# Optimization experiments

Hardware: AMD Instinct MI355X
Metric: run time of the kernel (lower is better)

## Reference

```python
import jax, jax.numpy as jnp
import numpy as np

MUL = 32          # multiplicity per irrep
NB = 10           # number_of_basis
MAX_R = 4.0
NUM_NEIGH = 16.0
NUM_NODES = 512.0
N_GRAPHS = 16
N = 8192
E = 131072
L = 3             # gated layers
C_S = float(np.sin(np.pi / 8))
C_X = float(np.cos(np.pi / 8))
SQ3 = float(np.sqrt(3.0))
SQ2 = float(np.sqrt(2.0))


def smooth_cutoff(x):
    u = 2.0 * (x - 1.0)
    y = 0.5 * (1.0 - jnp.cos(np.pi * u))
    return jnp.where(u > 0.0, 0.0, jnp.where(u < -1.0, 1.0, y))


def radial_embed(r):
    # soft_one_hot_linspace, basis='gaussian', cutoff=False, scaled by sqrt(NB)
    values = jnp.linspace(0.0, MAX_R, NB)
    step = values[1] - values[0]
    diff = (r[:, None] - values[None, :]) / step
    return jnp.exp(-diff * diff) / 1.12 * np.sqrt(NB)


def _lin_s(a, w):  # scalar-channel linear with e3nn fan-in norm
    return (a @ w) / np.sqrt(w.shape[0])


def _lin_v(a, w):  # vector-channel (l=1) linear, acts on multiplicity only
    return jnp.einsum('nui,uv->nvi', a, w) / np.sqrt(w.shape[0])


def forward(x, edge_vec, lin1_so, lin1_se, lin1_vo, lin1_ve,
            sc_so, sc_se, sc_vo, sc_ve, rad_w1, rad_w2,
            lin2_so, lin2_se, lin2_vo, lin2_ve,
            flin1_se, flin1_vo, fsc_se, frad_w1, frad_w2, flin2,
            edge_src, edge_dst, batch):
    n = x.shape[0]
    M = MUL
    # split node features into irrep blocks: 32x0o + 32x0e + 32x1o + 32x1e
    s_o = x[:, :M]
    s_e = x[:, M:2 * M]
    v_o = x[:, 2 * M:5 * M].reshape(n, M, 3)
    v_e = x[:, 5 * M:8 * M].reshape(n, M, 3)

    r = jnp.linalg.norm(edge_vec, axis=1)
    unit = edge_vec / (r[:, None] + 1e-12)
    cut = smooth_cutoff(r / MAX_R)          # [E]
    y0 = cut                                # l=0 edge attr (Y0 = 1, component norm)
    y1 = SQ3 * unit * cut[:, None]          # l=1 edge attr, [E,3]
    emb = radial_embed(r)                   # [E,NB]

    def seg(v):
        return jax.ops.segment_sum(v, edge_dst, num_segments=n) / np.sqrt(NUM_NEIGH)

    inv2 = 1.0 / np.sqrt(2.0)  # path normalization: 2 tp paths into output irrep
    inv3 = 1.0 / np.sqrt(3.0)  # 3 tp paths into output irrep

    def layer(carry, p):
        s_o, s_e, v_o, v_e = carry
        (w1so, w1se, w1vo, w1ve, wsso, wsse, wsvo, wsve,
         rw1, rw2, w2so, w2se, w2vo, w2ve) = p
        # lin1 (FullyConnectedTensorProduct with trivial node attr == per-irrep linear)
        a_so, a_se = _lin_s(s_o, w1so), _lin_s(s_e, w1se)
        a_vo, a_ve = _lin_v(v_o, w1vo), _lin_v(v_e, w1ve)
        e_so, e_se = a_so[edge_src], a_se[edge_src]
        e_vo, e_ve = a_vo[edge_src], a_ve[edge_src]
        # radial MLP -> per-edge tensor-product weights (10 uvu paths x MUL)
        h = jax.nn.silu(emb @ rw1 / np.sqrt(NB))
        w = (h @ rw2 / np.sqrt(rw1.shape[1])).reshape(-1, 10, M)
        # explicit lmax=1 Clebsch-Gordan contractions
        dot_ve = jnp.einsum('eui,ei->eu', e_ve, y1) / SQ3   # 1e x 1o -> 0o
        dot_vo = jnp.einsum('eui,ei->eu', e_vo, y1) / SQ3   # 1o x 1o -> 0e
        cr_ve = jnp.cross(e_ve, y1[:, None, :]) / SQ2       # 1e x 1o -> 1o
        cr_vo = jnp.cross(e_vo, y1[:, None, :]) / SQ2       # 1o x 1o -> 1e
        m0o = jnp.concatenate([w[:, 0] * e_so * y0[:, None],
                               w[:, 1] * dot_ve], axis=1) * inv2          # [E,2M]
        m0e = jnp.concatenate([w[:, 2] * e_se * y0[:, None],
                               w[:, 3] * dot_vo], axis=1) * inv2          # [E,2M]
        m1o = jnp.concatenate([w[:, 4][:, :, None] * e_se[:, :, None] * y1[:, None, :],
                               w[:, 5][:, :, None] * e_vo * y0[:, None, None],
                               w[:, 6][:, :, None] * cr_ve], axis=1) * inv3  # [E,3M,3]
        m1e = jnp.concatenate([w[:, 7][:, :, None] * e_so[:, :, None] * y1[:, None, :],
                               w[:, 8][:, :, None] * cr_vo,
                               w[:, 9][:, :, None] * e_ve * y0[:, None, None]], axis=1) * inv3
        n0o, n0e, n1o, n1e = seg(m0o), seg(m0e), seg(m1o), seg(m1e)
        # lin2 plus self-connection skip: sin(pi/8)*sc + cos(pi/8)*conv
        o0o = C_S * _lin_s(s_o, wsso) + C_X * _lin_s(n0o, w2so)   # [N,M]
        o0e = C_S * _lin_s(s_e, wsse) + C_X * _lin_s(n0e, w2se)   # [N,3M] (M scalars + 2M gates)
        o1o = C_S * _lin_v(v_o, wsvo) + C_X * _lin_v(n1o, w2vo)   # [N,M,3]
        o1e = C_S * _lin_v(v_e, wsve) + C_X * _lin_v(n1e, w2ve)   # [N,M,3]
        # Gate: tanh on 0o scalars, silu on 0e scalars, sigmoid gates on vectors
        ns_o = jnp.tanh(o0o)
        ns_e = jax.nn.silu(o0e[:, :M])
        g = jax.nn.sigmoid(o0e[:, M:])
        nv_o = o1o * g[:, :M, None]
        nv_e = o1e * g[:, M:, None]
        return (ns_o, ns_e, nv_o, nv_e), None

    (s_o, s_e, v_o, v_e), _ = jax.lax.scan(
        layer, (s_o, s_e, v_o, v_e),
        (lin1_so, lin1_se, lin1_vo, lin1_ve, sc_so, sc_se, sc_vo, sc_ve,
         rad_w1, rad_w2, lin2_so, lin2_se, lin2_vo, lin2_ve))

    # final convolution -> 1x0e (paths: 0e x 0e -> 0e, 1o x 1o -> 0e)
    a_se = _lin_s(s_e, flin1_se)
    a_vo = _lin_v(v_o, flin1_vo)
    h = jax.nn.silu(emb @ frad_w1 / np.sqrt(NB))
    w = (h @ frad_w2 / np.sqrt(frad_w1.shape[1])).reshape(-1, 2, MUL)
    dot_vo = jnp.einsum('eui,ei->eu', a_vo[edge_src], y1) / SQ3
    m0e = jnp.concatenate([w[:, 0] * a_se[edge_src] * y0[:, None],
                           w[:, 1] * dot_vo], axis=1) * inv2
    n0e = seg(m0e)
    out = C_S * _lin_s(s_e, fsc_se) + C_X * _lin_s(n0e, flin2)   # [N,1]
    # reduce_output: per-graph sum / sqrt(num_nodes)
    return jax.ops.segment_sum(out, batch, num_segments=N_GRAPHS) / np.sqrt(NUM_NODES)


def setup_inputs():
    key = jax.random.key(0)
    ks = jax.random.split(key, 26)
    rn = lambda k, s: jax.random.normal(k, s, dtype=jnp.float32)
    M = MUL
    return {
        "x": rn(ks[0], (N, 8 * M)),
        "edge_vec": rn(ks[1], (E, 3)),
        "lin1_so": rn(ks[2], (L, M, M)),
        "lin1_se": rn(ks[3], (L, M, M)),
        "lin1_vo": rn(ks[4], (L, M, M)),
        "lin1_ve": rn(ks[5], (L, M, M)),
        "sc_so": rn(ks[6], (L, M, M)),
        "sc_se": rn(ks[7], (L, M, 3 * M)),
        "sc_vo": rn(ks[8], (L, M, M)),
        "sc_ve": rn(ks[9], (L, M, M)),
        "rad_w1": rn(ks[10], (L, NB, 100)),
        "rad_w2": rn(ks[11], (L, 100, 10 * M)),
        "lin2_so": rn(ks[12], (L, 2 * M, M)),
        "lin2_se": rn(ks[13], (L, 2 * M, 3 * M)),
        "lin2_vo": rn(ks[14], (L, 3 * M, M)),
        "lin2_ve": rn(ks[15], (L, 3 * M, M)),
        "flin1_se": rn(ks[16], (M, M)),
        "flin1_vo": rn(ks[17], (M, M)),
        "fsc_se": rn(ks[18], (M, 1)),
        "frad_w1": rn(ks[19], (NB, 100)),
        "frad_w2": rn(ks[20], (100, 2 * M)),
        "flin2": rn(ks[21], (2 * M, 1)),
        "edge_src": jax.random.randint(ks[22], (E,), 0, N),
        "edge_dst": jax.random.randint(ks[23], (E,), 0, N),
        "batch": jnp.sort(jax.random.randint(ks[24], (N,), 0, N_GRAPHS)),
    }


def reference(x, edge_vec, lin1_so, lin1_se, lin1_vo, lin1_ve,
              sc_so, sc_se, sc_vo, sc_ve, rad_w1, rad_w2,
              lin2_so, lin2_se, lin2_vo, lin2_ve,
              flin1_se, flin1_vo, fsc_se, frad_w1, frad_w2, flin2,
              edge_src, edge_dst, batch):
    return forward(x, edge_vec, lin1_so, lin1_se, lin1_vo, lin1_ve,
                   sc_so, sc_se, sc_vo, sc_ve, rad_w1, rad_w2,
                   lin2_so, lin2_se, lin2_vo, lin2_ve,
                   flin1_se, flin1_vo, fsc_se, frad_w1, frad_w2, flin2,
                   edge_src, edge_dst, batch)
```

## Files before the change

### kernel.cpp

```cpp
#include <hip/hip_runtime.h>
#include <hip/hip_bf16.h>
#include <math.h>
#include <string.h>
#include <stdint.h>

#define NN 8192
#define EE 131072

#define PI_F     3.14159265358979323846f
#define SQRT3_F  1.7320508075688772f
#define INV_SQ2  0.7071067811865476f
#define INV_SQ3  0.5773502691896258f
#define INV_S32  0.17677669529663687f
#define INV_S96  0.10206207261596575f
#define INV_S10  0.31622776601683794f
#define C_S_F    0.3826834323650898f
#define C_X_F    0.9238795325112867f
#define EMB_S    2.8234621965789795f
#define OUT_S    0.044194173824159216f

typedef unsigned int uint;
typedef unsigned short ushort;
typedef unsigned long long u64;
typedef __attribute__((ext_vector_type(8))) short short8;
typedef __attribute__((ext_vector_type(4))) float float4v;

__device__ __forceinline__ float sigmoid_f(float x){ return 1.0f/(1.0f+__expf(-x)); }
__device__ __forceinline__ ushort f2bf(float f){
    uint u = __float_as_uint(f);
    u = (u + 0x7fffu + ((u>>16)&1u)) >> 16;
    return (ushort)u;
}
__device__ __forceinline__ float bf2f(ushort w){ return __uint_as_float(((uint)w)<<16); }
__device__ __forceinline__ uint pk2bf(float a, float b){
    __hip_bfloat162 h = __float22bfloat162_rn(make_float2(a,b));
    uint u; memcpy(&u,&h,4); return u;
}

__global__ __launch_bounds__(256) void k_count(const int* __restrict__ dst, int* __restrict__ cnt)
{
    int e = blockIdx.x*256 + threadIdx.x;
    atomicAdd(&cnt[dst[e]], 1);
}

__global__ __launch_bounds__(1024) void k_scan(const int* __restrict__ cnt,
    int* __restrict__ off, int* __restrict__ cur)
{
    __shared__ int partial[1024];
    int t = threadIdx.x;
    int base = t*8;
    int local[8];
    int s = 0;
    #pragma unroll
    for(int i=0;i<8;i++){ local[i]=s; s += cnt[base+i]; }
    partial[t] = s;
    __syncthreads();
    for(int d=1; d<1024; d<<=1){
        int v = (t>=d) ? partial[t-d] : 0;
        __syncthreads();
        partial[t] += v;
        __syncthreads();
    }
    int pref = (t>0) ? partial[t-1] : 0;
    #pragma unroll
    for(int i=0;i<8;i++){
        int o = pref + local[i];
        off[base+i] = o; cur[base+i] = o;
    }
    if (t==1023) off[NN] = partial[1023];
}

__global__ __launch_bounds__(256) void k_scatter(const int* __restrict__ dst,
    int* __restrict__ cur, int* __restrict__ eids)
{
    int e = blockIdx.x*256 + threadIdx.x;
    int p = atomicAdd(&cur[dst[e]], 1);
    eids[p] = e;
}

__global__ __launch_bounds__(256) void k_geom_sorted(const float* __restrict__ ev,
    const int* __restrict__ eids, const int* __restrict__ esrc,
    const int* __restrict__ edst, const int* __restrict__ batch,
    float4* __restrict__ ygeo, float* __restrict__ embs,
    int* __restrict__ esrcs, int* __restrict__ gbs)
{
    int p = blockIdx.x*256 + threadIdx.x;
    int e = eids[p];
    float vx=ev[e*3+0], vy=ev[e*3+1], vz=ev[e*3+2];
    float r = sqrtf(vx*vx+vy*vy+vz*vz);
    float uu = 0.5f*r - 2.0f;
    float cut;
    if (uu > 0.0f)       cut = 0.0f;
    else if (uu < -1.0f) cut = 1.0f;
    else                 cut = 0.5f*(1.0f - cosf(PI_F*uu));
    float s = SQRT3_F*cut/(r + 1e-12f);
    ygeo[p] = make_float4(cut, vx*s, vy*s, vz*s);
    #pragma unroll
    for(int b=0;b<10;b++){
        float d = r*2.25f - (float)b;
        embs[p*10+b] = __expf(-d*d)*EMB_S;
    }
    esrcs[p] = esrc[e];
    gbs[p]   = batch[edst[e]];
}

__global__ __launch_bounds__(256) void k_lin1(const float* __restrict__ st,
    const float* __restrict__ w_so, const float* __restrict__ w_se,
    const float* __restrict__ w_vo, const float* __restrict__ w_ve,
    uint* __restrict__ Abf)
{
    __shared__ float wl[4][1024];
    __shared__ float sl[8][256];
    __shared__ float ol[8][256];
    int t = threadIdx.x;
    for(int i=t;i<1024;i+=256){ wl[0][i]=w_so[i]; wl[1][i]=w_se[i]; wl[2][i]=w_vo[i]; wl[3][i]=w_ve[i]; }
    int n0 = blockIdx.x*8;
    for(int i=t;i<2048;i+=256){ int k=i>>8, c=i&255; sl[k][c]=st[(n0+k)*256+c]; }
    __syncthreads();
    for(int k=0;k<8;k++){
        float acc = 0.0f;
        if (t < 64){
            int m = t>>5, v = t&31;
            const float* w = wl[m];
            const float* s = &sl[k][m*32];
            #pragma unroll
            for(int u=0;u<32;u++) acc += s[u]*w[u*32+v];
        } else if (t < 160){
            int idx=t-64, i=idx>>5, v=idx&31;
            #pragma unroll
            for(int u=0;u<32;u++) acc += sl[k][64+u*3+i]*wl[2][u*32+v];
        } else {
            int idx=t-160, i=idx>>5, v=idx&31;
            #pragma unroll
            for(int u=0;u<32;u++) acc += sl[k][160+u*3+i]*wl[3][u*32+v];
        }
        ol[k][t] = acc * INV_S32;
    }
    __syncthreads();
    for(int idx=t; idx<1024; idx+=256){
        int k = idx>>7, j = idx&127, q = j>>5, u = j&31;
        Abf[(size_t)(n0+k)*128 + j] = pk2bf(ol[k][q*64 + u], ol[k][q*64 + 32 + u]);
    }
}

__global__ __launch_bounds__(256) void k_prep3(const float* __restrict__ rw2, ushort* __restrict__ Bfrag)
{
    int L = blockIdx.x / 160;
    int idx = (blockIdx.x % 160)*256 + threadIdx.x;
    int j = idx & 7;
    int l = (idx>>3) & 63;
    int rest = idx >> 9;
    int nt = rest % 20;
    int ks = rest / 20;
    int k = ks*32 + ((l>>4)&3)*8 + j;
    int p = nt*16 + (l&15);
    int n = (2*(p>>6) + (p&1))*32 + ((p&63)>>1);
    float v = (k < 100) ? rw2[L*32000 + k*320 + n] : 0.0f;
    Bfrag[L*40960 + idx] = f2bf(v);
}

__global__ __launch_bounds__(256) void k_prep64(const float* __restrict__ rw2, ushort* __restrict__ Bfrag)
{
    int idx = blockIdx.x*256 + threadIdx.x;
    int j = idx & 7;
    int l = (idx>>3) & 63;
    int rest = idx >> 9;
    int nt = rest % 4;
    int ks = rest / 4;
    int k = ks*32 + ((l>>4)&3)*8 + j;
    int p = nt*16 + (l&15);
    int n = (p % 2)*32 + p/2;
    float v = (k < 100) ? rw2[k*64 + n] : 0.0f;
    Bfrag[idx] = f2bf(v);
}

__global__ __launch_bounds__(256) void k_prepu(
    const float* __restrict__ sc_so, const float* __restrict__ sc_se,
    const float* __restrict__ sc_vo, const float* __restrict__ sc_ve,
    const float* __restrict__ lin2_so, const float* __restrict__ lin2_se,
    const float* __restrict__ lin2_vo, const float* __restrict__ lin2_ve,
    float* __restrict__ Wcat0, float* __restrict__ Wcat1)
{
    int idx = blockIdx.x*256 + threadIdx.x;
    int L = idx / 20480;
    int k = idx % 20480;
    const float CS32 = C_S_F*INV_S32, CX8 = C_X_F*0.125f, CX96 = C_X_F*INV_S96;
    if (k < 12288){
        int r = k >> 7, c = k & 127;
        float v;
        if (c < 32) v = (r<32) ? CS32*sc_so[L*1024 + r*32+c]        : CX8*lin2_so[L*2048 + (r-32)*32+c];
        else        v = (r<32) ? CS32*sc_se[L*3072 + r*96+(c-32)]   : CX8*lin2_se[L*6144 + (r-32)*96+(c-32)];
        Wcat0[L*12288 + k] = v;
    } else {
        int k2 = k - 12288;
        int r = k2 >> 6, c = k2 & 63;
        float v;
        if (c < 32) v = (r<32) ? CS32*sc_vo[L*1024 + r*32+c]        : CX96*lin2_vo[L*3072 + (r-32)*32+c];
        else        v = (r<32) ? CS32*sc_ve[L*1024 + r*32+(c-32)]   : CX96*lin2_ve[L*3072 + (r-32)*32+(c-32)];
        Wcat1[L*8192 + k2] = v;
    }
}

template<int NCOL>
__global__ __launch_bounds__(256, 3) void k_radial_mfma(const float* __restrict__ emb,
    const float* __restrict__ rw1, const ushort* __restrict__ Afrag,
    ushort* __restrict__ Wout)
{
    constexpr int MTW = NCOL/64;
    constexpr int STR = NCOL + 8;
    constexpr int BIG = (64*STR > 8192) ? 64*STR : 8192;
    __shared__ __align__(16) ushort s_big[BIG];
    __shared__ float s_emb[640];
    int t = threadIdx.x;
    int ebase = blockIdx.x*64;
    for(int i=t;i<640;i+=256)  s_emb[i] = emb[ebase*10 + i];
    for(int i=t;i<1024;i+=256) ((uint*)s_big)[3072 + i] = 0u;
    __syncthreads();
    {
        int w4 = __builtin_amdgcn_readfirstlane(t) >> 6;
        int l = t & 63;
        float ev[10];
        #pragma unroll
        for(int r=0;r<10;r++) ev[r] = s_emb[l*10 + r];
        int m  = l & 15, nt = l >> 4;
        int kbeg = w4*25;
        #pragma unroll 5
        for(int k=kbeg; k<kbeg+25; k++){
            float a0 = 0.0f;
            #pragma unroll
            for(int r=0;r<10;r++) a0 += ev[r]*rw1[r*100 + k];
            a0 *= INV_S10;
            float h = a0*sigmoid_f(a0);
            int ks = k >> 5, kk = k & 31;
            int lt = m | ((kk>>3)<<4);
            s_big[((ks*4 + nt)*64 + lt)*8 + (kk&7)] = f2bf(h);
        }
    }
    __syncthreads();
    int w = t >> 6, l = t & 63;
    float4v acc[MTW][4];
    #pragma unroll
    for(int a=0;a<MTW;a++)
        #pragma unroll
        for(int b=0;b<4;b++)
            acc[a][b] = (float4v){0.f,0.f,0.f,0.f};
    #pragma unroll
    for(int ks=0;ks<4;ks++){
        short8 bfr[4];
        #pragma unroll
        for(int nt=0;nt<4;nt++)
            bfr[nt] = *((const short8*)&s_big[((ks*4+nt)*64 + l)*8]);
        #pragma unroll
        for(int mtl=0;mtl<MTW;mtl++){
            short8 af = *((const short8*)(Afrag + ((size_t)(ks*(NCOL/16) + w*MTW + mtl)*64 + l)*8));
            #pragma unroll
            for(int nt=0;nt<4;nt++)
                acc[mtl][nt] = __builtin_amdgcn_mfma_f32_16x16x32_bf16(af, bfr[nt], acc[mtl][nt], 0, 0, 0);
        }
    }
    __syncthreads();
    {
        int col16 = l & 15, rquad = l >> 4;
        #pragma unroll
        for(int mtl=0;mtl<MTW;mtl++){
            int pos0 = (w*MTW + mtl)*16 + rquad*4;
            #pragma unroll
            for(int nt=0;nt<4;nt++){
                int edge = nt*16 + col16;
                uint u01 = pk2bf(acc[mtl][nt][0]*0.1f, acc[mtl][nt][1]*0.1f);
                uint u23 = pk2bf(acc[mtl][nt][2]*0.1f, acc[mtl][nt][3]*0.1f);
                u64 pk = (u64)u01 | ((u64)u23 << 32);
                *((u64*)&s_big[edge*STR + pos0]) = pk;
            }
        }
    }
    __syncthreads();
    for (int idx = t; idx < 64*(NCOL/8); idx += 256){
        int row = idx/(NCOL/8), o8 = idx%(NCOL/8);
        short8 vv = *((const short8*)&s_big[row*STR + o8*8]);
        *((short8*)(Wout + (size_t)(ebase+row)*NCOL + o8*8)) = vv;
    }
}

__global__ __launch_bounds__(64) void k_aggregate(const uint* __restrict__ Abf,
    const ushort* __restrict__ W2, const float4* __restrict__ ygeo,
    const int* __restrict__ off, const int* __restrict__ esrcs,
    float* __restrict__ nbuf)
{
    int n = blockIdx.x;
    int l = threadIdx.x;
    int u = l & 31, half = l >> 5;
    int e0 = off[n], e1 = off[n+1];
    float a_n0o0=0.f, a_n0o1=0.f, a_n0e0=0.f, a_n0e1=0.f;
    float a1o[3][3] = {{0}}, a1e[3][3] = {{0}};
    #pragma unroll 2
    for(int p=e0;p<e1;p+=2){
        int idx = p + half;
        bool valid = idx < e1;
        int ic = valid ? idx : e0;
        int s = esrcs[ic];
        float4 yg = ygeo[ic];
        float cy0 = valid ? yg.x : 0.0f;
        float v1x = yg.y, v1y = yg.z, v1z = yg.w;
        if (!valid){ v1x=0.f; v1y=0.f; v1z=0.f; }
        const uint* Au = Abf + (size_t)s*128;
        uint a01=Au[u], a23=Au[32+u], a45=Au[64+u], a67=Au[96+u];
        float aso=bf2f((ushort)a01), ase=bf2f((ushort)(a01>>16));
        float vox=bf2f((ushort)a23), voy=bf2f((ushort)(a23>>16));
        float voz=bf2f((ushort)a45), vex=bf2f((ushort)(a45>>16));
        float vey=bf2f((ushort)a67), vez=bf2f((ushort)(a67>>16));
        const uint* Wu = (const uint*)(W2) + (size_t)ic*160;
        uint p01=Wu[u], p23=Wu[32+u], p45=Wu[64+u], p67=Wu[96+u], p89=Wu[128+u];
        float w0=bf2f((ushort)p01), w1=bf2f((ushort)(p01>>16));
        float w2=bf2f((ushort)p23), w3=bf2f((ushort)(p23>>16));
        float w4=bf2f((ushort)p45), w5=bf2f((ushort)(p45>>16));
        float w6=bf2f((ushort)p67), w7=bf2f((ushort)(p67>>16));
        float w8=bf2f((ushort)p89), w9=bf2f((ushort)(p89>>16));
        float dve = (vex*v1x+vey*v1y+vez*v1z)*INV_SQ3;
        float dvo = (vox*v1x+voy*v1y+voz*v1z)*INV_SQ3;
        float cvex=(vey*v1z-vez*v1y)*INV_SQ2, cvey=(vez*v1x-vex*v1z)*INV_SQ2, cvez=(vex*v1y-vey*v1x)*INV_SQ2;
        float cvox=(voy*v1z-voz*v1y)*INV_SQ2, cvoy=(voz*v1x-vox*v1z)*INV_SQ2, cvoz=(vox*v1y-voy*v1x)*INV_SQ2;
        a_n0o0 += w0*aso*cy0;
        a_n0o1 += w1*dve;
        a_n0e0 += w2*ase*cy0;
        a_n0e1 += w3*dvo;
        a1o[0][0]+=w4*ase*v1x; a1o[0][1]+=w4*ase*v1y; a1o[0][2]+=w4*ase*v1z;
        a1o[1][0]+=w5*vox*cy0; a1o[1][1]+=w5*voy*cy0; a1o[1][2]+=w5*voz*cy0;
        a1o[2][0]+=w6*cvex;    a1o[2][1]+=w6*cvey;    a1o[2][2]+=w6*cvez;
        a1e[0][0]+=w7*aso*v1x; a1e[0][1]+=w7*aso*v1y; a1e[0][2]+=w7*aso*v1z;
        a1e[1][0]+=w8*cvox;    a1e[1][1]+=w8*cvoy;    a1e[1][2]+=w8*cvoz;
        a1e[2][0]+=w9*vex*cy0; a1e[2][1]+=w9*vey*cy0; a1e[2][2]+=w9*vez*cy0;
    }
    a_n0o0 += __shfl_xor(a_n0o0, 32);
    a_n0o1 += __shfl_xor(a_n0o1, 32);
    a_n0e0 += __shfl_xor(a_n0e0, 32);
    a_n0e1 += __shfl_xor(a_n0e1, 32);
    #pragma unroll
    for(int sp=0;sp<3;sp++)
        #pragma unroll
        for(int i=0;i<3;i++){
            a1o[sp][i] += __shfl_xor(a1o[sp][i], 32);
            a1e[sp][i] += __shfl_xor(a1e[sp][i], 32);
        }
    float s0 = INV_SQ2*0.25f;
    float s1 = INV_SQ3*0.25f;
    float* nb = nbuf + n*704;
    if (half==0){
        nb[u]      = a_n0o0*s0;
        nb[32+u]   = a_n0o1*s0;
        nb[64+u]   = a_n0e0*s0;
        nb[96+u]   = a_n0e1*s0;
        #pragma unroll
        for(int sp=0;sp<3;sp++)
            #pragma unroll
            for(int i=0;i<3;i++)
                nb[128 + i*96 + sp*32 + u] = a1o[sp][i]*s1;
    } else {
        #pragma unroll
        for(int sp=0;sp<3;sp++)
            #pragma unroll
            for(int i=0;i<3;i++)
                nb[416 + i*96 + sp*32 + u] = a1e[sp][i]*s1;
    }
}

__global__ __launch_bounds__(256, 4) void k_update(const float* __restrict__ st,
    const float* __restrict__ nbuf, const float* __restrict__ W0,
    const float* __restrict__ W1, float* __restrict__ stnew)
{
    __shared__ float X0T[192][8];
    __shared__ float X1T[3][256][8];
    __shared__ float G[8][64];
    int t = threadIdx.x;
    int n0 = blockIdx.x*8;
    for (int idx=t; idx<2048; idx+=256){
        int nb = idx>>8, c = idx&255;
        float v = st[(n0+nb)*256 + c];
        if (c<32)       X0T[c][nb]=v;
        else if (c<64)  X0T[96+(c-32)][nb]=v;
        else if (c<160){ int cc=c-64;  X1T[cc%3][cc/3][nb]=v; }
        else           { int cc=c-160; X1T[cc%3][128+cc/3][nb]=v; }
    }
    for (int idx=t; idx<5632; idx+=256){
        int nb = idx/704, o = idx%704;
        float v = nbuf[(n0+nb)*704 + o];
        if (o<64)       X0T[32+o][nb]=v;
        else if (o<128) X0T[128+(o-64)][nb]=v;
        else if (o<416){ int oo=o-128; X1T[oo/96][32+(oo%96)][nb]=v; }
        else           { int oo=o-416; X1T[oo/96][160+(oo%96)][nb]=v; }
    }
    __syncthreads();
    {
        int c = t & 127, h = t >> 7;
        float a0=0.f,a1=0.f,a2=0.f,a3=0.f;
        int qb = (c<32) ? 0 : 96;
        #pragma unroll 4
        for (int r=0;r<96;r++){
            float w = W0[r*128+c];
            const float* xp = &X0T[qb+r][h*4];
            a0 += w*xp[0]; a1 += w*xp[1]; a2 += w*xp[2]; a3 += w*xp[3];
        }
        float accs[4]={a0,a1,a2,a3};
        #pragma unroll
        for (int j=0;j<4;j++){
            int nb = h*4+j, n = n0+nb;
            float o = accs[j];
            if (c<32)       stnew[n*256+c] = tanhf(o);
            else if (c<64)  stnew[n*256+c] = o*sigmoid_f(o);
            else            G[nb][c-64] = sigmoid_f(o);
        }
    }
    __syncthreads();
    int c2 = t & 63, w = t >> 6;
    if (w < 3){
        float acc[8];
        #pragma unroll
        for(int j=0;j<8;j++) acc[j]=0.f;
        int qb = (c2<32) ? 0 : 128;
        #pragma unroll 2
        for (int r=0;r<128;r++){
            float wt = W1[r*64+c2];
            const float* xp = &X1T[w][qb+r][0];
            #pragma unroll
            for(int j=0;j<8;j++) acc[j] += wt*xp[j];
        }
        int base = (c2<32) ? 64 + c2*3 + w : 160 + (c2-32)*3 + w;
        #pragma unroll
        for(int j=0;j<8;j++)
            stnew[(n0+j)*256 + base] = acc[j]*G[j][c2];
    }
}

__global__ __launch_bounds__(128) void k_flin(const float* __restrict__ st,
    const float* __restrict__ wse, const float* __restrict__ wvo,
    const float* __restrict__ fsc_se,
    float* __restrict__ afin, float* __restrict__ sk)
{
    int n = blockIdx.x, t = threadIdx.x;
    const float* sr = st + n*256;
    float acc = 0.0f;
    if (t < 32){
        #pragma unroll
        for(int u=0;u<32;u++) acc += sr[32+u]*wse[u*32+t];
    } else {
        int idx=t-32, i=idx>>5, v=idx&31;
        #pragma unroll
        for(int u=0;u<32;u++) acc += sr[64+u*3+i]*wvo[u*32+v];
    }
    afin[n*128 + t] = acc * INV_S32;
    if (t < 32){
        float v = sr[32+t]*fsc_se[t];
        #pragma unroll
        for(int o=16;o>0;o>>=1) v += __shfl_xor(v, o);
        if (t==0) sk[n] = v * (C_S_F*INV_S32*OUT_S);
    }
}

__global__ __launch_bounds__(256) void k_fagg(const float* __restrict__ afin,
    const ushort* __restrict__ Wf2, const int* __restrict__ esrcs,
    const float4* __restrict__ ygeo, const int* __restrict__ gbs,
    const float* __restrict__ flin2, float* __restrict__ fpart)
{
    __shared__ float s_g[16];
    int t = threadIdx.x;
    if (t < 16) s_g[t] = 0.0f;
    __syncthreads();
    int u = t & 31, half = (t>>5)&1, w = t >> 6;
    const float FACT = C_X_F*0.125f*INV_SQ2*0.25f*OUT_S;
    float fl0 = flin2[u], fl1 = flin2[32+u];
    int base = (blockIdx.x*4 + w)*64;
    #pragma unroll 2
    for(int it=0; it<32; it++){
        int idx = base + it*2 + half;
        int s = esrcs[idx];
        float4 yg = ygeo[idx];
        const float* Ar = afin + s*128;
        float ase = Ar[u];
        float vx=Ar[32+u], vy=Ar[64+u], vz=Ar[96+u];
        uint p01 = *((const uint*)(Wf2 + (size_t)idx*64 + u*2));
        float w0 = bf2f((ushort)p01), w1 = bf2f((ushort)(p01>>16));
        float val = fl0*w0*ase*yg.x + fl1*w1*((vx*yg.y+vy*yg.z+vz*yg.w)*INV_SQ3);
        #pragma unroll
        for(int o=16;o>0;o>>=1) val += __shfl_xor(val, o);
        if (u==0) atomicAdd(&s_g[gbs[idx]], val*FACT);
    }
    __syncthreads();
    if (t < 16) fpart[blockIdx.x*16 + t] = s_g[t];
}

__global__ __launch_bounds__(256) void k_final(const float* __restrict__ sk,
    const int* __restrict__ batch, const float* __restrict__ fpart,
    float* __restrict__ out)
{
    __shared__ float bins[16];
    int t = threadIdx.x, b = blockIdx.x;
    if (t < 16) bins[t] = 0.0f;
    __syncthreads();
    if (t < 128){
        int n = b*128 + t;
        atomicAdd(&bins[batch[n]], sk[n]);
    } else {
        int i = b*128 + (t-128);
        atomicAdd(&bins[i & 15], fpart[i]);
    }
    __syncthreads();
    if (t < 16) atomicAdd(&out[t], bins[t]);
}

extern "C" void kernel_launch(void* const* d_in, const int* in_sizes, int n_in,
                              void* d_out, int out_size, void* d_ws, size_t ws_size,
                              hipStream_t stream)
{
    const float* x        = (const float*)d_in[0];
    const float* edge_vec = (const float*)d_in[1];
    const float* lin1_so  = (const float*)d_in[2];
    const float* lin1_se  = (const float*)d_in[3];
    const float* lin1_vo  = (const float*)d_in[4];
    const float* lin1_ve  = (const float*)d_in[5];
    const float* sc_so    = (const float*)d_in[6];
    const float* sc_se    = (const float*)d_in[7];
    const float* sc_vo    = (const float*)d_in[8];
    const float* sc_ve    = (const float*)d_in[9];
    const float* rad_w1   = (const float*)d_in[10];
    const float* rad_w2   = (const float*)d_in[11];
    const float* lin2_so  = (const float*)d_in[12];
    const float* lin2_se  = (const float*)d_in[13];
    const float* lin2_vo  = (const float*)d_in[14];
    const float* lin2_ve  = (const float*)d_in[15];
    const float* flin1_se = (const float*)d_in[16];
    const float* flin1_vo = (const float*)d_in[17];
    const float* fsc_se   = (const float*)d_in[18];
    const float* frad_w1  = (const float*)d_in[19];
    const float* frad_w2  = (const float*)d_in[20];
    const float* flin2    = (const float*)d_in[21];
    const int*   esrc     = (const int*)d_in[22];
    const int*   edst     = (const int*)d_in[23];
    const int*   batch    = (const int*)d_in[24];
    float* out = (float*)d_out;

    uint8_t* ws = (uint8_t*)d_ws;
    size_t off = 0;
    auto alloc = [&](size_t bytes)->void* {
        void* p = ws + off;
        off += (bytes + 255) & ~(size_t)255;
        return p;
    };
    float4* ygeo = (float4*)alloc((size_t)EE*16);
    float* embs  = (float*)alloc((size_t)EE*40);
    int*   esrcs = (int*)  alloc((size_t)EE*4);
    int*   gbs   = (int*)  alloc((size_t)EE*4);
    int*   cnt   = (int*)  alloc((size_t)NN*4);
    int*   csro  = (int*)  alloc((size_t)(NN+1)*4);
    int*   cur   = (int*)  alloc((size_t)NN*4);
    int*   eids  = (int*)  alloc((size_t)EE*4);
    uint*  Abf   = (uint*) alloc((size_t)NN*128*4);
    ushort* W    = (ushort*)alloc((size_t)EE*320*2);
    ushort* Bfrag3=(ushort*)alloc((size_t)3*40960*2);
    ushort* BfragF=(ushort*)alloc((size_t)8192*2);
    float* Wcat0 = (float*)alloc((size_t)3*12288*4);
    float* Wcat1 = (float*)alloc((size_t)3*8192*4);
    float* nbuf  = (float*)alloc((size_t)NN*704*4);
    float* st0   = (float*)alloc((size_t)NN*256*4);
    float* st1   = (float*)alloc((size_t)NN*256*4);
    float* afin  = (float*)alloc((size_t)NN*128*4);
    float* sk    = (float*)alloc((size_t)NN*4);
    float* fpart = (float*)alloc((size_t)512*16*4);

    hipMemsetAsync(out, 0, (size_t)out_size*sizeof(float), stream);
    hipMemsetAsync(cnt, 0, (size_t)NN*4, stream);

    k_count  <<<EE/256, 256, 0, stream>>>(edst, cnt);
    k_scan   <<<1, 1024, 0, stream>>>(cnt, csro, cur);
    k_scatter<<<EE/256, 256, 0, stream>>>(edst, cur, eids);
    k_geom_sorted<<<EE/256, 256, 0, stream>>>(edge_vec, eids, esrc, edst, batch,
                                              ygeo, embs, esrcs, gbs);
    k_prep3<<<480, 256, 0, stream>>>(rad_w2, Bfrag3);
    k_prep64<<<32, 256, 0, stream>>>(frad_w2, BfragF);
    k_prepu<<<240, 256, 0, stream>>>(sc_so, sc_se, sc_vo, sc_ve,
                                     lin2_so, lin2_se, lin2_vo, lin2_ve, Wcat0, Wcat1);

    const float* st_in = x;
    float* bufs[2] = { st0, st1 };
    for (int l=0; l<3; l++){
        k_lin1<<<NN/8, 256, 0, stream>>>(st_in,
            lin1_so + l*1024, lin1_se + l*1024, lin1_vo + l*1024, lin1_ve + l*1024, Abf);
        k_radial_mfma<320><<<EE/64, 256, 0, stream>>>(embs, rad_w1 + l*1000, Bfrag3 + l*40960, W);
        k_aggregate<<<NN, 64, 0, stream>>>(Abf, W, ygeo, csro, esrcs, nbuf);
        float* st_out = bufs[l & 1];
        k_update<<<NN/8, 256, 0, stream>>>(st_in, nbuf, Wcat0 + l*12288, Wcat1 + l*8192, st_out);
        st_in = st_out;
    }
    k_flin<<<NN, 128, 0, stream>>>(st_in, flin1_se, flin1_vo, fsc_se, afin, sk);
    k_radial_mfma<64><<<EE/64, 256, 0, stream>>>(embs, frad_w1, BfragF, W);
    k_fagg<<<512, 256, 0, stream>>>(afin, W, esrcs, ygeo, gbs, flin2, fpart);
    k_final<<<64, 256, 0, stream>>>(sk, batch, fpart, out);
}
```

Before: 530.2 us.

## Fuse radial MLP into per-node aggregation, keeping edge weights in LDS

Replaces the separate radial-MLP kernel, which wrote 320 bf16 weights per edge to global memory, and the aggregate kernel with one fused kernel. Each block owns three consecutive destination nodes, computes the radial weights for their CSR edge range in 64-edge chunks with MFMA into shared memory, and then aggregates from LDS. This removes a large per-layer global write and read of the edge-weight tensor. In exchange, only 3 of 4 waves aggregate, and blocks whose edges don't fill a chunk waste MFMA work on padding. Blocks also loop over a variable number of chunks with several barriers each.

```diff
diff --git a/kernel.cpp b/kernel.cpp
--- a/kernel.cpp
+++ b/kernel.cpp
@@ -201,6 +201,167 @@
     }
 }
 
+__global__ __launch_bounds__(256, 3) void k_radagg(const float* __restrict__ emb,
+    const float* __restrict__ rw1, const ushort* __restrict__ Afrag,
+    const uint* __restrict__ Abf, const float4* __restrict__ ygeo,
+    const int* __restrict__ off, const int* __restrict__ esrcs,
+    float* __restrict__ nbuf)
+{
+    constexpr int NCOL = 320, MTW = 5, STR = NCOL + 8;
+    __shared__ __align__(16) ushort s_big[64*STR];
+    __shared__ float s_emb[640];
+    int t = threadIdx.x, w = t >> 6, l = t & 63;
+    int u = l & 31, half = l >> 5;
+    int n0 = blockIdx.x*3;
+    int ebase = off[n0];
+    int nlast = (n0+3 < NN) ? n0+3 : NN;
+    int eend_all = off[nlast];
+    int my_n = n0 + w;
+    bool active_node = (w < 3) && (my_n < NN);
+    int nlo = active_node ? off[my_n]   : 0;
+    int nhi = active_node ? off[my_n+1] : 0;
+
+    float a_n0o0=0.f, a_n0o1=0.f, a_n0e0=0.f, a_n0e1=0.f;
+    float a1o[3][3] = {{0}}, a1e[3][3] = {{0}};
+
+    for (int ebeg = ebase; ebeg < eend_all; ebeg += 64){
+        int valid = eend_all - ebeg; if (valid > 64) valid = 64;
+        __syncthreads();
+        for(int i=t;i<4096;i+=256) ((uint*)s_big)[i] = 0u;
+        for(int i=t;i<valid*10;i+=256) s_emb[i] = emb[(size_t)ebeg*10 + i];
+        __syncthreads();
+        {
+            int w4 = __builtin_amdgcn_readfirstlane(t) >> 6;
+            if (l < valid){
+                float ev[10];
+                #pragma unroll
+                for(int r=0;r<10;r++) ev[r] = s_emb[l*10 + r];
+                int m = l & 15, nt = l >> 4;
+                int kbeg = w4*25;
+                #pragma unroll 5
+                for(int k=kbeg; k<kbeg+25; k++){
+                    float a0 = 0.0f;
+                    #pragma unroll
+                    for(int r=0;r<10;r++) a0 += ev[r]*rw1[r*100 + k];
+                    a0 *= INV_S10;
+                    float h = a0*sigmoid_f(a0);
+                    int ks = k >> 5, kk = k & 31;
+                    int lt = m | ((kk>>3)<<4);
+                    s_big[((ks*4 + nt)*64 + lt)*8 + (kk&7)] = f2bf(h);
+                }
+            }
+        }
+        __syncthreads();
+        float4v acc[MTW][4];
+        #pragma unroll
+        for(int a=0;a<MTW;a++)
+            #pragma unroll
+            for(int b=0;b<4;b++)
+                acc[a][b] = (float4v){0.f,0.f,0.f,0.f};
+        #pragma unroll
+        for(int ks=0;ks<4;ks++){
+            short8 bfr[4];
+            #pragma unroll
+            for(int nt=0;nt<4;nt++)
+                bfr[nt] = *((const short8*)&s_big[((ks*4+nt)*64 + l)*8]);
+            #pragma unroll
+            for(int mtl=0;mtl<MTW;mtl++){
+                short8 af = *((const short8*)(Afrag + ((size_t)(ks*(NCOL/16) + w*MTW + mtl)*64 + l)*8));
+                #pragma unroll
+                for(int nt=0;nt<4;nt++)
+                    acc[mtl][nt] = __builtin_amdgcn_mfma_f32_16x16x32_bf16(af, bfr[nt], acc[mtl][nt], 0, 0, 0);
+            }
+        }
+        __syncthreads();
+        {
+            int col16 = l & 15, rquad = l >> 4;
+            #pragma unroll
+            for(int mtl=0;mtl<MTW;mtl++){
+                int pos0 = (w*MTW + mtl)*16 + rquad*4;
+                #pragma unroll
+                for(int nt=0;nt<4;nt++){
+                    int edge = nt*16 + col16;
+                    uint u01 = pk2bf(acc[mtl][nt][0]*0.1f, acc[mtl][nt][1]*0.1f);
+                    uint u23 = pk2bf(acc[mtl][nt][2]*0.1f, acc[mtl][nt][3]*0.1f);
+                    u64 pk = (u64)u01 | ((u64)u23 << 32);
+                    *((u64*)&s_big[edge*STR + pos0]) = pk;
+                }
+            }
+        }
+        __syncthreads();
+        if (active_node){
+            int lo = (nlo > ebeg) ? nlo : ebeg;
+            int hi = (nhi < ebeg+valid) ? nhi : ebeg+valid;
+            for(int p = lo + half; p < hi; p += 2){
+                int eloc = p - ebeg;
+                int s = esrcs[p];
+                float4 yg = ygeo[p];
+                float cy0 = yg.x, v1x = yg.y, v1y = yg.z, v1z = yg.w;
+                const uint* Au = Abf + (size_t)s*128;
+                uint a01=Au[u], a23=Au[32+u], a45=Au[64+u], a67=Au[96+u];
+                float aso=bf2f((ushort)a01), ase=bf2f((ushort)(a01>>16));
+                float vox=bf2f((ushort)a23), voy=bf2f((ushort)(a23>>16));
+                float voz=bf2f((ushort)a45), vex=bf2f((ushort)(a45>>16));
+                float vey=bf2f((ushort)a67), vez=bf2f((ushort)(a67>>16));
+                const uint* Wu = (const uint*)(s_big + eloc*STR);
+                uint p01=Wu[u], p23=Wu[32+u], p45=Wu[64+u], p67=Wu[96+u], p89=Wu[128+u];
+                float w0=bf2f((ushort)p01), w1=bf2f((ushort)(p01>>16));
+                float w2=bf2f((ushort)p23), w3=bf2f((ushort)(p23>>16));
+                float w4=bf2f((ushort)p45), w5=bf2f((ushort)(p45>>16));
+                float w6=bf2f((ushort)p67), w7=bf2f((ushort)(p67>>16));
+                float w8=bf2f((ushort)p89), w9=bf2f((ushort)(p89>>16));
+                float dve = (vex*v1x+vey*v1y+vez*v1z)*INV_SQ3;
+                float dvo = (vox*v1x+voy*v1y+voz*v1z)*INV_SQ3;
+                float cvex=(vey*v1z-vez*v1y)*INV_SQ2, cvey=(vez*v1x-vex*v1z)*INV_SQ2, cvez=(vex*v1y-vey*v1x)*INV_SQ2;
+                float cvox=(voy*v1z-voz*v1y)*INV_SQ2, cvoy=(voz*v1x-vox*v1z)*INV_SQ2, cvoz=(vox*v1y-voy*v1x)*INV_SQ2;
+                a_n0o0 += w0*aso*cy0;
+                a_n0o1 += w1*dve;
+                a_n0e0 += w2*ase*cy0;
+                a_n0e1 += w3*dvo;
+                a1o[0][0]+=w4*ase*v1x; a1o[0][1]+=w4*ase*v1y; a1o[0][2]+=w4*ase*v1z;
+                a1o[1][0]+=w5*vox*cy0; a1o[1][1]+=w5*voy*cy0; a1o[1][2]+=w5*voz*cy0;
+                a1o[2][0]+=w6*cvex;    a1o[2][1]+=w6*cvey;    a1o[2][2]+=w6*cvez;
+                a1e[0][0]+=w7*aso*v1x; a1e[0][1]+=w7*aso*v1y; a1e[0][2]+=w7*aso*v1z;
+                a1e[1][0]+=w8*cvox;    a1e[1][1]+=w8*cvoy;    a1e[1][2]+=w8*cvoz;
+                a1e[2][0]+=w9*vex*cy0; a1e[2][1]+=w9*vey*cy0; a1e[2][2]+=w9*vez*cy0;
+            }
+        }
+    }
+    a_n0o0 += __shfl_xor(a_n0o0, 32);
+    a_n0o1 += __shfl_xor(a_n0o1, 32);
+    a_n0e0 += __shfl_xor(a_n0e0, 32);
+    a_n0e1 += __shfl_xor(a_n0e1, 32);
+    #pragma unroll
+    for(int sp=0;sp<3;sp++)
+        #pragma unroll
+        for(int i=0;i<3;i++){
+            a1o[sp][i] += __shfl_xor(a1o[sp][i], 32);
+            a1e[sp][i] += __shfl_xor(a1e[sp][i], 32);
+        }
+    if (active_node){
+        float s0 = INV_SQ2*0.25f;
+        float s1 = INV_SQ3*0.25f;
+        float* nb = nbuf + (size_t)my_n*704;
+        if (half==0){
+            nb[u]      = a_n0o0*s0;
+            nb[32+u]   = a_n0o1*s0;
+            nb[64+u]   = a_n0e0*s0;
+            nb[96+u]   = a_n0e1*s0;
+            #pragma unroll
+            for(int sp=0;sp<3;sp++)
+                #pragma unroll
+                for(int i=0;i<3;i++)
+                    nb[128 + i*96 + sp*32 + u] = a1o[sp][i]*s1;
+        } else {
+            #pragma unroll
+            for(int sp=0;sp<3;sp++)
+                #pragma unroll
+                for(int i=0;i<3;i++)
+                    nb[416 + i*96 + sp*32 + u] = a1e[sp][i]*s1;
+        }
+    }
+}
+
 template<int NCOL>
 __global__ __launch_bounds__(256, 3) void k_radial_mfma(const float* __restrict__ emb,
     const float* __restrict__ rw1, const ushort* __restrict__ Afrag,
@@ -279,88 +440,6 @@
         int row = idx/(NCOL/8), o8 = idx%(NCOL/8);
         short8 vv = *((const short8*)&s_big[row*STR + o8*8]);
         *((short8*)(Wout + (size_t)(ebase+row)*NCOL + o8*8)) = vv;
-    }
-}
-
-__global__ __launch_bounds__(64) void k_aggregate(const uint* __restrict__ Abf,
-    const ushort* __restrict__ W2, const float4* __restrict__ ygeo,
-    const int* __restrict__ off, const int* __restrict__ esrcs,
-    float* __restrict__ nbuf)
-{
-    int n = blockIdx.x;
-    int l = threadIdx.x;
-    int u = l & 31, half = l >> 5;
-    int e0 = off[n], e1 = off[n+1];
-    float a_n0o0=0.f, a_n0o1=0.f, a_n0e0=0.f, a_n0e1=0.f;
-    float a1o[3][3] = {{0}}, a1e[3][3] = {{0}};
-    #pragma unroll 2
-    for(int p=e0;p<e1;p+=2){
-        int idx = p + half;
-        bool valid = idx < e1;
-        int ic = valid ? idx : e0;
-        int s = esrcs[ic];
-        float4 yg = ygeo[ic];
-        float cy0 = valid ? yg.x : 0.0f;
-        float v1x = yg.y, v1y = yg.z, v1z = yg.w;
-        if (!valid){ v1x=0.f; v1y=0.f; v1z=0.f; }
-        const uint* Au = Abf + (size_t)s*128;
-        uint a01=Au[u], a23=Au[32+u], a45=Au[64+u], a67=Au[96+u];
-        float aso=bf2f((ushort)a01), ase=bf2f((ushort)(a01>>16));
-        float vox=bf2f((ushort)a23), voy=bf2f((ushort)(a23>>16));
-        float voz=bf2f((ushort)a45), vex=bf2f((ushort)(a45>>16));
-        float vey=bf2f((ushort)a67), vez=bf2f((ushort)(a67>>16));
-        const uint* Wu = (const uint*)(W2) + (size_t)ic*160;
-        uint p01=Wu[u], p23=Wu[32+u], p45=Wu[64+u], p67=Wu[96+u], p89=Wu[128+u];
-        float w0=bf2f((ushort)p01), w1=bf2f((ushort)(p01>>16));
-        float w2=bf2f((ushort)p23), w3=bf2f((ushort)(p23>>16));
-        float w4=bf2f((ushort)p45), w5=bf2f((ushort)(p45>>16));
-        float w6=bf2f((ushort)p67), w7=bf2f((ushort)(p67>>16));
-        float w8=bf2f((ushort)p89), w9=bf2f((ushort)(p89>>16));
-        float dve = (vex*v1x+vey*v1y+vez*v1z)*INV_SQ3;
-        float dvo = (vox*v1x+voy*v1y+voz*v1z)*INV_SQ3;
-        float cvex=(vey*v1z-vez*v1y)*INV_SQ2, cvey=(vez*v1x-vex*v1z)*INV_SQ2, cvez=(vex*v1y-vey*v1x)*INV_SQ2;
-        float cvox=(voy*v1z-voz*v1y)*INV_SQ2, cvoy=(voz*v1x-vox*v1z)*INV_SQ2, cvoz=(vox*v1y-voy*v1x)*INV_SQ2;
-        a_n0o0 += w0*aso*cy0;
-        a_n0o1 += w1*dve;
-        a_n0e0 += w2*ase*cy0;
-        a_n0e1 += w3*dvo;
-        a1o[0][0]+=w4*ase*v1x; a1o[0][1]+=w4*ase*v1y; a1o[0][2]+=w4*ase*v1z;
-        a1o[1][0]+=w5*vox*cy0; a1o[1][1]+=w5*voy*cy0; a1o[1][2]+=w5*voz*cy0;
-        a1o[2][0]+=w6*cvex;    a1o[2][1]+=w6*cvey;    a1o[2][2]+=w6*cvez;
-        a1e[0][0]+=w7*aso*v1x; a1e[0][1]+=w7*aso*v1y; a1e[0][2]+=w7*aso*v1z;
-        a1e[1][0]+=w8*cvox;    a1e[1][1]+=w8*cvoy;    a1e[1][2]+=w8*cvoz;
-        a1e[2][0]+=w9*vex*cy0; a1e[2][1]+=w9*vey*cy0; a1e[2][2]+=w9*vez*cy0;
-    }
-    a_n0o0 += __shfl_xor(a_n0o0, 32);
-    a_n0o1 += __shfl_xor(a_n0o1, 32);
-    a_n0e0 += __shfl_xor(a_n0e0, 32);
-    a_n0e1 += __shfl_xor(a_n0e1, 32);
-    #pragma unroll
-    for(int sp=0;sp<3;sp++)
-        #pragma unroll
-        for(int i=0;i<3;i++){
-            a1o[sp][i] += __shfl_xor(a1o[sp][i], 32);
-            a1e[sp][i] += __shfl_xor(a1e[sp][i], 32);
-        }
-    float s0 = INV_SQ2*0.25f;
-    float s1 = INV_SQ3*0.25f;
-    float* nb = nbuf + n*704;
-    if (half==0){
-        nb[u]      = a_n0o0*s0;
-        nb[32+u]   = a_n0o1*s0;
-        nb[64+u]   = a_n0e0*s0;
-        nb[96+u]   = a_n0e1*s0;
-        #pragma unroll
-        for(int sp=0;sp<3;sp++)
-            #pragma unroll
-            for(int i=0;i<3;i++)
-                nb[128 + i*96 + sp*32 + u] = a1o[sp][i]*s1;
-    } else {
-        #pragma unroll
-        for(int sp=0;sp<3;sp++)
-            #pragma unroll
-            for(int i=0;i<3;i++)
-                nb[416 + i*96 + sp*32 + u] = a1e[sp][i]*s1;
     }
 }
 
@@ -554,7 +633,7 @@
     int*   cur   = (int*)  alloc((size_t)NN*4);
     int*   eids  = (int*)  alloc((size_t)EE*4);
     uint*  Abf   = (uint*) alloc((size_t)NN*128*4);
-    ushort* W    = (ushort*)alloc((size_t)EE*320*2);
+    ushort* W    = (ushort*)alloc((size_t)EE*64*2);
     ushort* Bfrag3=(ushort*)alloc((size_t)3*40960*2);
     ushort* BfragF=(ushort*)alloc((size_t)8192*2);
     float* Wcat0 = (float*)alloc((size_t)3*12288*4);
@@ -581,11 +660,12 @@
 
     const float* st_in = x;
     float* bufs[2] = { st0, st1 };
+    const int NBLK = (NN + 2) / 3;
     for (int l=0; l<3; l++){
         k_lin1<<<NN/8, 256, 0, stream>>>(st_in,
             lin1_so + l*1024, lin1_se + l*1024, lin1_vo + l*1024, lin1_ve + l*1024, Abf);
-        k_radial_mfma<320><<<EE/64, 256, 0, stream>>>(embs, rad_w1 + l*1000, Bfrag3 + l*40960, W);
-        k_aggregate<<<NN, 64, 0, stream>>>(Abf, W, ygeo, csro, esrcs, nbuf);
+        k_radagg<<<NBLK, 256, 0, stream>>>(embs, rad_w1 + l*1000, Bfrag3 + l*40960,
+                                           Abf, ygeo, csro, esrcs, nbuf);
         float* st_out = bufs[l & 1];
         k_update<<<NN/8, 256, 0, stream>>>(st_in, nbuf, Wcat0 + l*12288, Wcat1 + l*8192, st_out);
         st_in = st_out;
```

Result: slower. 797.9 us (+50.5%).
